# Kernel optimization log

Hardware: AMD Instinct MI355X
Metric: run time of the kernel (lower is better)

Reference implementation:

```python
import jax, jax.numpy as jnp
import numpy as np

N, E, ND, ED, HD = 50000, 800000, 64, 64, 192  # HD == 2*ND + ED (required by edge_gru)
NEG_SLOPE_BOOST = 0.2   # LeakyReLU inside msg_booster
NEG_SLOPE_OUT = 0.01    # F.leaky_relu default
LN_EPS = 1e-5


def leaky_relu(x, slope):
    return jnp.where(x > 0, x, slope * x)


def msg_booster(x, W1, b1, ln_g, ln_b, W2, b2):
    # Linear -> LayerNorm -> LeakyReLU(0.2) -> Linear
    y = x @ W1.T + b1
    mu = jnp.mean(y, axis=-1, keepdims=True)
    var = jnp.var(y, axis=-1, keepdims=True)
    y = (y - mu) * jax.lax.rsqrt(var + LN_EPS) * ln_g + ln_b
    y = leaky_relu(y, NEG_SLOPE_BOOST)
    return y @ W2.T + b2


def gru_cell(x, h, Wih, Whh, bih, bhh):
    gi = x @ Wih.T + bih
    gh = h @ Whh.T + bhh
    ir, iz, inn = jnp.split(gi, 3, axis=-1)
    hr, hz, hn = jnp.split(gh, 3, axis=-1)
    r = jax.nn.sigmoid(ir + hr)
    z = jax.nn.sigmoid(iz + hz)
    n = jnp.tanh(inn + r * hn)
    return (1.0 - z) * n + z * h


def setup_inputs() -> dict:
    key = jax.random.key(0)
    ks = jax.random.split(key, 24)
    r = lambda i, shape: jax.random.normal(ks[i], shape, dtype=jnp.float32) * 0.05
    return dict(
        node_feats=jax.random.normal(ks[0], (N, ND), dtype=jnp.float32),
        edge_feats=jax.random.normal(ks[1], (E, ED), dtype=jnp.float32),
        src=jax.random.randint(ks[2], (E,), 0, N),
        dst=jax.random.randint(ks[3], (E,), 0, N),
        W1e=r(4, (HD, 2 * ND + ED)),       # booster first linear, edge path
        W1n=r(5, (HD, 2 * (ND + ED))),     # booster first linear, node path
        b1=r(6, (HD,)),
        ln_g=jnp.ones((HD,), jnp.float32),
        ln_b=jnp.zeros((HD,), jnp.float32),
        W2=r(7, (HD, HD)), b2=r(8, (HD,)),
        Wih_e=r(9, (3 * ED, HD)), Whh_e=r(10, (3 * ED, ED)),
        bih_e=r(11, (3 * ED,)), bhh_e=r(12, (3 * ED,)),
        Wih_a=r(13, (3 * ND, HD)), Whh_a=r(14, (3 * ND, ND)),
        bih_a=r(15, (3 * ND,)), bhh_a=r(16, (3 * ND,)),
        Wre=r(17, (ED, ED)), bre=r(18, (ED,)),
        Wra=r(19, (ND, ND)), bra=r(20, (ND,)),
    )


def reference(node_feats, edge_feats, src, dst,
              W1e, W1n, b1, ln_g, ln_b, W2, b2,
              Wih_e, Whh_e, bih_e, bhh_e,
              Wih_a, Whh_a, bih_a, bhh_a,
              Wre, bre, Wra, bra):
    # --- edge update: gather src/dst node feats, concat with edge feats ---
    h_src = node_feats[src]                       # [E, ND]
    h_dst = node_feats[dst]                       # [E, ND]
    msg = jnp.concatenate([h_src, h_dst, edge_feats], axis=1)  # [E, 2ND+ED]
    edge_input = msg_booster(msg, W1e, b1, ln_g, ln_b, W2, b2)  # [E, HD]
    update_edges = leaky_relu(
        gru_cell(edge_input, edge_feats, Wih_e, Whh_e, bih_e, bhh_e)
        + edge_feats @ Wre.T + bre, NEG_SLOPE_OUT)              # [E, ED]

    # --- message passing: m = [h_src, e'] aggregated at dst by sum and max ---
    m = jnp.concatenate([h_src, update_edges], axis=1)          # [E, ND+ED]
    agg_sum = jax.ops.segment_sum(m, dst, num_segments=N)       # [N, ND+ED]
    agg_max = jax.ops.segment_max(m, dst, num_segments=N)
    agg_max = jnp.where(jnp.isfinite(agg_max), agg_max, 0.0)    # empty mailbox -> 0
    agg = jnp.concatenate([agg_sum, agg_max], axis=1)           # [N, 2(ND+ED)]

    node_input = msg_booster(agg, W1n, b1, ln_g, ln_b, W2, b2)  # [N, HD]
    update_nodes = leaky_relu(
        gru_cell(node_input, node_feats, Wih_a, Whh_a, bih_a, bhh_a)
        + node_feats @ Wra.T + bra, NEG_SLOPE_OUT)              # [N, ND]
    return update_nodes, update_edges
```

## Files before the change

### kernel.cpp

```cpp
#include <hip/hip_runtime.h>

#define NN 50000
#define EE 800000
#define ND 64
#define ED 64
#define HD 192
#define AS 196

typedef short s16x8 __attribute__((ext_vector_type(8)));
typedef float f32x4 __attribute__((ext_vector_type(4)));

#define MFMA16 __builtin_amdgcn_mfma_f32_16x16x32_bf16

__device__ __forceinline__ unsigned short bf16rn(float x) {
  unsigned u = __float_as_uint(x);
  return (unsigned short)((u + 0x7fffu + ((u >> 16) & 1u)) >> 16);
}

__device__ __forceinline__ void split8(const float* p, s16x8& hi, s16x8& lo) {
  f32x4 a = *(const f32x4*)p;
  f32x4 b = *(const f32x4*)(p + 4);
#pragma unroll
  for (int j = 0; j < 4; ++j) {
    unsigned short h = bf16rn(a[j]);
    float hf = __uint_as_float(((unsigned)h) << 16);
    unsigned short l = bf16rn(a[j] - hf);
    hi[j] = (short)h; lo[j] = (short)l;
  }
#pragma unroll
  for (int j = 0; j < 4; ++j) {
    unsigned short h = bf16rn(b[j]);
    float hf = __uint_as_float(((unsigned)h) << 16);
    unsigned short l = bf16rn(b[j] - hf);
    hi[4 + j] = (short)h; lo[4 + j] = (short)l;
  }
}

__device__ __forceinline__ float fsigmoid(float x) { return 1.f / (1.f + __expf(-x)); }
__device__ __forceinline__ float ftanh(float x) {
  const float ax = fabsf(x);
  const float t = __expf(2.f * ax);
  const float r = 1.f - 2.f / (t + 1.f);
  return x >= 0.f ? r : -r;
}

template <int NT, int KS, int NTOT = NT>
__device__ __forceinline__ void gemm3p(f32x4* acc, const s16x8* ah, const s16x8* al,
                                       const unsigned short* __restrict__ pack, int lane) {
  const int HOFF = NTOT * KS * 512;
#pragma unroll
  for (int ks = 0; ks < KS; ++ks) {
#pragma unroll
    for (int nt = 0; nt < NT; ++nt) {
      const unsigned short* bp = pack + ((nt * KS + ks) * 64 + lane) * 8;
      s16x8 bh = *(const s16x8*)bp;
      s16x8 bl = *(const s16x8*)(bp + HOFF);
      acc[nt] = MFMA16(ah[ks], bh, acc[nt], 0, 0, 0);
      acc[nt] = MFMA16(al[ks], bh, acc[nt], 0, 0, 0);
      acc[nt] = MFMA16(ah[ks], bl, acc[nt], 0, 0, 0);
    }
  }
}

__global__ void k_pack(const float* __restrict__ w0, const float* __restrict__ w1,
                       const float* __restrict__ w2, const float* __restrict__ w3,
                       const float* __restrict__ w4, const float* __restrict__ w5,
                       const float* __restrict__ w6, const float* __restrict__ w7,
                       const float* __restrict__ w8, unsigned short* __restrict__ packs) {
  int gid = blockIdx.x * 256 + threadIdx.x;
  const float* w; int off, sz, KS, K, local;
  if      (gid <  36864) { w = w0; off = 0;      sz = 36864; KS = 6; K = 192; local = gid; }
  else if (gid <  86016) { w = w1; off = 73728;  sz = 49152; KS = 8; K = 256; local = gid - 36864; }
  else if (gid < 122880) { w = w2; off = 172032; sz = 36864; KS = 6; K = 192; local = gid - 86016; }
  else if (gid < 159744) { w = w3; off = 245760; sz = 36864; KS = 6; K = 192; local = gid - 122880; }
  else if (gid < 172032) { w = w4; off = 319488; sz = 12288; KS = 2; K = 64;  local = gid - 159744; }
  else if (gid < 176128) { w = w5; off = 344064; sz = 4096;  KS = 2; K = 64;  local = gid - 172032; }
  else if (gid < 212992) { w = w6; off = 352256; sz = 36864; KS = 6; K = 192; local = gid - 176128; }
  else if (gid < 225280) { w = w7; off = 425984; sz = 12288; KS = 2; K = 64;  local = gid - 212992; }
  else                   { w = w8; off = 450560; sz = 4096;  KS = 2; K = 64;  local = gid - 225280; }
  int j = local & 7;
  int lane = (local >> 3) & 63;
  int t = local >> 9;
  int ks = t % KS, nt = t / KS;
  int n = nt * 16 + (lane & 15);
  int k = ks * 32 + ((lane >> 4) & 3) * 8 + j;
  float v = w[n * K + k];
  unsigned short h = bf16rn(v);
  float hf = __uint_as_float(((unsigned)h) << 16);
  unsigned short l = bf16rn(v - hf);
  packs[off + local] = h;
  packs[off + sz + local] = l;
}

__global__ void k_packfuse(const float* __restrict__ W2,
                           const float* __restrict__ WihE, const float* __restrict__ WihA,
                           unsigned short* __restrict__ packs) {
  int gid = blockIdx.x * 256 + threadIdx.x;
  const float* Wih; int off, local;
  if (gid < 36864) { Wih = WihE; off = 245760; local = gid; }
  else             { Wih = WihA; off = 352256; local = gid - 36864; }
  int j = local & 7;
  int lane = (local >> 3) & 63;
  int t = local >> 9;
  int ks = t % 6, nt = t / 6;
  int n = nt * 16 + (lane & 15);
  int k = ks * 32 + ((lane >> 4) & 3) * 8 + j;
  const float* wr = Wih + n * HD;
  float acc = 0.f;
#pragma unroll 4
  for (int jj = 0; jj < HD; ++jj) acc = fmaf(wr[jj], W2[jj * HD + k], acc);
  unsigned short h = bf16rn(acc);
  float hf = __uint_as_float(((unsigned)h) << 16);
  unsigned short l = bf16rn(acc - hf);
  packs[off + local] = h;
  packs[off + 36864 + local] = l;
}

__global__ void k_fusebias(const float* __restrict__ WihE, const float* __restrict__ WihA,
                           const float* __restrict__ b2, const float* __restrict__ bihE,
                           const float* __restrict__ bihA, float* __restrict__ bf) {
  int i = threadIdx.x;
  const float* Wih = (i < 192) ? WihE : WihA;
  const float* bih = (i < 192) ? bihE : bihA;
  int n = (i < 192) ? i : i - 192;
  float acc = bih[n];
  for (int k = 0; k < HD; ++k) acc = fmaf(Wih[n * HD + k], b2[k], acc);
  bf[i] = acc;
}

__global__ void k_zero(int* __restrict__ cnt) {
  int i = blockIdx.x * 256 + threadIdx.x;
  if (i < NN) cnt[i] = 0;
}
__global__ void k_hist(const int* __restrict__ dst, int* __restrict__ cnt) {
  int e = blockIdx.x * 256 + threadIdx.x;
  if (e < EE) atomicAdd(&cnt[dst[e]], 1);
}
__global__ void k_scan(const int* __restrict__ cnt, int* __restrict__ roff, int* __restrict__ cursor) {
  __shared__ int wsum[16];
  const int tid = threadIdx.x;
  const int lane = tid & 63, wid = tid >> 6;
  int carry = 0;
  for (int c = 0; c < 49; ++c) {
    const int idx = c * 1024 + tid;
    const int v = (idx < NN) ? cnt[idx] : 0;
    int x = v;
#pragma unroll
    for (int off = 1; off < 64; off <<= 1) {
      int y = __shfl_up(x, off, 64);
      if (lane >= off) x += y;
    }
    if (lane == 63) wsum[wid] = x;
    __syncthreads();
    if (wid == 0 && lane < 16) {
      int s = wsum[lane];
#pragma unroll
      for (int off = 1; off < 16; off <<= 1) {
        int y = __shfl_up(s, off, 16);
        if (lane >= off) s += y;
      }
      wsum[lane] = s;
    }
    __syncthreads();
    const int wbase = (wid == 0) ? 0 : wsum[wid - 1];
    const int excl = carry + wbase + x - v;
    if (idx < NN) { roff[idx] = excl; cursor[idx] = excl; }
    const int total = wsum[15];
    __syncthreads();
    carry += total;
  }
  if (tid == 0) roff[NN] = carry;
}
__global__ void k_scatter(const int* __restrict__ dst, int* __restrict__ cursor, int* __restrict__ elist) {
  int e = blockIdx.x * 256 + threadIdx.x;
  if (e < EE) {
    int p = atomicAdd(&cursor[dst[e]], 1);
    elist[p] = e;
  }
}

__global__ __launch_bounds__(256, 3)
void edge_kernel(const float* __restrict__ nf, const float* __restrict__ efg,
                 const int* __restrict__ src, const int* __restrict__ dst,
                 const float* __restrict__ b1, const float* __restrict__ lng,
                 const float* __restrict__ lnb,
                 const float* __restrict__ bfz, const float* __restrict__ bhh,
                 const float* __restrict__ bre,
                 const unsigned short* __restrict__ pW1,
                 const unsigned short* __restrict__ pWih, const unsigned short* __restrict__ pWhh,
                 const unsigned short* __restrict__ pWre,
                 float* __restrict__ oute) {
  __shared__ float act[64 * AS];
  const int tid = threadIdx.x;
  const int e0 = blockIdx.x * 64;

  {
    const int r = tid >> 2, q = tid & 3;
    const int s = src[e0 + r];
    const int d = dst[e0 + r];
    const f32x4* nf4 = (const f32x4*)nf;
    const f32x4* ef4 = (const f32x4*)efg;
#pragma unroll
    for (int i = 0; i < 4; ++i) {
      const int c4 = q * 4 + i;
      *(f32x4*)&act[r * AS + c4 * 4]       = nf4[s * 16 + c4];
      *(f32x4*)&act[r * AS + 64 + c4 * 4]  = nf4[d * 16 + c4];
      *(f32x4*)&act[r * AS + 128 + c4 * 4] = ef4[(e0 + r) * 16 + c4];
    }
  }
  __syncthreads();

  const int w = tid >> 6, lane = tid & 63;
  const int quad = lane >> 4, lc = lane & 15;
  const int arow = w * 16 + lc;
  const int obase = w * 16 + quad * 4;
  const f32x4 vzero = {0.f, 0.f, 0.f, 0.f};

  s16x8 ah[6], al[6];
  f32x4 acc[12];

#pragma unroll
  for (int ks = 0; ks < 6; ++ks) split8(&act[arow * AS + ks * 32 + quad * 8], ah[ks], al[ks]);
#pragma unroll
  for (int nt = 0; nt < 12; ++nt) acc[nt] = vzero;
  gemm3p<12, 6>(acc, ah, al, pW1, lane);
  {
    float s1[4] = {0, 0, 0, 0}, s2[4] = {0, 0, 0, 0};
#pragma unroll
    for (int nt = 0; nt < 12; ++nt) {
      const float bb = b1[nt * 16 + lc];
#pragma unroll
      for (int r = 0; r < 4; ++r) {
        const float v = acc[nt][r] + bb;
        acc[nt][r] = v; s1[r] += v; s2[r] += v * v;
      }
    }
#pragma unroll
    for (int r = 0; r < 4; ++r) {
#pragma unroll
      for (int m = 1; m < 16; m <<= 1) {
        s1[r] += __shfl_xor(s1[r], m, 16);
        s2[r] += __shfl_xor(s2[r], m, 16);
      }
      const float mu = s1[r] * (1.f / 192.f);
      const float va = s2[r] * (1.f / 192.f) - mu * mu;
      s1[r] = mu; s2[r] = rsqrtf(va + 1e-5f);
    }
#pragma unroll
    for (int nt = 0; nt < 12; ++nt) {
      const int col = nt * 16 + lc;
      const float g = lng[col], be = lnb[col];
#pragma unroll
      for (int r = 0; r < 4; ++r) {
        float v = (acc[nt][r] - s1[r]) * s2[r] * g + be;
        v = v > 0.f ? v : 0.2f * v;
        act[(obase + r) * AS + col] = v;
      }
    }
  }
  __syncthreads();

#pragma unroll
  for (int ks = 0; ks < 6; ++ks) split8(&act[arow * AS + ks * 32 + quad * 8], ah[ks], al[ks]);
  f32x4 rz[8], ni[4], nh[4], ro[4];
#pragma unroll
  for (int nt = 0; nt < 8; ++nt) rz[nt] = vzero;
#pragma unroll
  for (int nt = 0; nt < 4; ++nt) { ni[nt] = vzero; nh[nt] = vzero; ro[nt] = vzero; }
  gemm3p<8, 6, 12>(rz, ah, al, pWih, lane);
  gemm3p<4, 6, 12>(ni, ah, al, pWih + 8 * 6 * 512, lane);

  s16x8 eh[2], el[2];
#pragma unroll
  for (int ks = 0; ks < 2; ++ks)
    split8(efg + (size_t)(e0 + arow) * ED + ks * 32 + quad * 8, eh[ks], el[ks]);
  gemm3p<8, 2, 12>(rz, eh, el, pWhh, lane);
  gemm3p<4, 2, 12>(nh, eh, el, pWhh + 8 * 2 * 512, lane);
  gemm3p<4, 2>(ro, eh, el, pWre, lane);

#pragma unroll
  for (int nt = 0; nt < 4; ++nt) {
    const int col = nt * 16 + lc;
    const float bir = bfz[col], biz = bfz[64 + col], bin = bfz[128 + col];
    const float bhr = bhh[col], bhz = bhh[64 + col], bhn = bhh[128 + col];
    const float br = bre[col];
#pragma unroll
    for (int r = 0; r < 4; ++r) {
      const int row = obase + r;
      const float h = efg[(size_t)(e0 + row) * ED + col];
      const float rg = fsigmoid(rz[nt][r] + bir + bhr);
      const float zg = fsigmoid(rz[nt + 4][r] + biz + bhz);
      const float ng = ftanh(ni[nt][r] + bin + rg * (nh[nt][r] + bhn));
      float v = (1.f - zg) * ng + zg * h + ro[nt][r] + br;
      v = v > 0.f ? v : 0.01f * v;
      oute[(size_t)(e0 + row) * ED + col] = v;
    }
  }
}

__global__ __launch_bounds__(256, 2)
void node_kernel(const float* __restrict__ nf,
                 const int* __restrict__ src,
                 const int* __restrict__ roff, const int* __restrict__ elist,
                 const float* __restrict__ b1, const float* __restrict__ lng,
                 const float* __restrict__ lnb,
                 const float* __restrict__ bfz, const float* __restrict__ bhh,
                 const float* __restrict__ bra,
                 const unsigned short* __restrict__ pW1,
                 const unsigned short* __restrict__ pWih, const unsigned short* __restrict__ pWhh,
                 const unsigned short* __restrict__ pWra,
                 const float* __restrict__ upd,
                 float* __restrict__ outn) {
  __shared__ float act[4 * 4096];
  const int tid = threadIdx.x;
  const int w = tid >> 6, lane = tid & 63;
  const int nb0 = blockIdx.x * 64;
  float* win = act + w * 4096;

  {
    const int half = lane >> 5, c2 = (lane & 31) * 2;
#pragma unroll 1
    for (int i = 0; i < 16; ++i) {
      const int node = nb0 + w * 16 + i;
      float s0 = 0.f, s1v = 0.f;
      float m0 = -__builtin_inff(), m1 = -__builtin_inff();
      if (node < NN) {
        const int sidx = roff[node], eidx = roff[node + 1];
        int ix = sidx;
        for (; ix + 1 < eidx; ix += 2) {
          const int ea = elist[ix], eb = elist[ix + 1];
          const float* pa = half ? (upd + (size_t)ea * ED + c2) : (nf + (size_t)src[ea] * ND + c2);
          const float* pb = half ? (upd + (size_t)eb * ED + c2) : (nf + (size_t)src[eb] * ND + c2);
          const float a0 = pa[0], a1 = pa[1], c0 = pb[0], c1 = pb[1];
          s0 += a0 + c0; s1v += a1 + c1;
          m0 = fmaxf(m0, fmaxf(a0, c0)); m1 = fmaxf(m1, fmaxf(a1, c1));
        }
        if (ix < eidx) {
          const int ea = elist[ix];
          const float* pa = half ? (upd + (size_t)ea * ED + c2) : (nf + (size_t)src[ea] * ND + c2);
          const float a0 = pa[0], a1 = pa[1];
          s0 += a0; s1v += a1;
          m0 = fmaxf(m0, a0); m1 = fmaxf(m1, a1);
        }
        if (sidx == eidx) { m0 = 0.f; m1 = 0.f; }
      } else {
        m0 = 0.f; m1 = 0.f;
      }
      const int cs = half * 64 + c2;
      win[i * 256 + cs] = s0;
      win[i * 256 + cs + 1] = s1v;
      win[i * 256 + 128 + cs] = m0;
      win[i * 256 + 128 + cs + 1] = m1;
    }
  }
  __syncthreads();

  const int quad = lane >> 4, lc = lane & 15;
  const f32x4 vzero = {0.f, 0.f, 0.f, 0.f};

  s16x8 ah8[8], al8[8];
#pragma unroll
  for (int ks = 0; ks < 8; ++ks) split8(&win[lc * 256 + ks * 32 + quad * 8], ah8[ks], al8[ks]);
  f32x4 acc[12];
#pragma unroll
  for (int nt = 0; nt < 12; ++nt) acc[nt] = vzero;
  gemm3p<12, 8>(acc, ah8, al8, pW1, lane);
  {
    float s1[4] = {0, 0, 0, 0}, s2[4] = {0, 0, 0, 0};
#pragma unroll
    for (int nt = 0; nt < 12; ++nt) {
      const float bb = b1[nt * 16 + lc];
#pragma unroll
      for (int r = 0; r < 4; ++r) {
        const float v = acc[nt][r] + bb;
        acc[nt][r] = v; s1[r] += v; s2[r] += v * v;
      }
    }
#pragma unroll
    for (int r = 0; r < 4; ++r) {
#pragma unroll
      for (int m = 1; m < 16; m <<= 1) {
        s1[r] += __shfl_xor(s1[r], m, 16);
        s2[r] += __shfl_xor(s2[r], m, 16);
      }
      const float mu = s1[r] * (1.f / 192.f);
      const float va = s2[r] * (1.f / 192.f) - mu * mu;
      s1[r] = mu; s2[r] = rsqrtf(va + 1e-5f);
    }
#pragma unroll
    for (int nt = 0; nt < 12; ++nt) {
      const int col = nt * 16 + lc;
      const float g = lng[col], be = lnb[col];
#pragma unroll
      for (int r = 0; r < 4; ++r) {
        float v = (acc[nt][r] - s1[r]) * s2[r] * g + be;
        v = v > 0.f ? v : 0.2f * v;
        win[(quad * 4 + r) * AS + col] = v;
      }
    }
  }
  __syncthreads();

  s16x8 ah[6], al[6];
#pragma unroll
  for (int ks = 0; ks < 6; ++ks) split8(&win[lc * AS + ks * 32 + quad * 8], ah[ks], al[ks]);
  f32x4 rz[8], ni[4], nh[4], ro[4];
#pragma unroll
  for (int nt = 0; nt < 8; ++nt) rz[nt] = vzero;
#pragma unroll
  for (int nt = 0; nt < 4; ++nt) { ni[nt] = vzero; nh[nt] = vzero; ro[nt] = vzero; }
  gemm3p<8, 6, 12>(rz, ah, al, pWih, lane);
  gemm3p<4, 6, 12>(ni, ah, al, pWih + 8 * 6 * 512, lane);

  s16x8 hh[2], hl[2];
  {
    const int gr = nb0 + w * 16 + lc;
    const float* hp = nf + (size_t)(gr < NN ? gr : NN - 1) * ND;
#pragma unroll
    for (int ks = 0; ks < 2; ++ks) split8(hp + ks * 32 + quad * 8, hh[ks], hl[ks]);
  }
  gemm3p<8, 2, 12>(rz, hh, hl, pWhh, lane);
  gemm3p<4, 2, 12>(nh, hh, hl, pWhh + 8 * 2 * 512, lane);
  gemm3p<4, 2>(ro, hh, hl, pWra, lane);

#pragma unroll
  for (int nt = 0; nt < 4; ++nt) {
    const int col = nt * 16 + lc;
    const float bir = bfz[col], biz = bfz[64 + col], bin = bfz[128 + col];
    const float bhr = bhh[col], bhz = bhh[64 + col], bhn = bhh[128 + col];
    const float br = bra[col];
#pragma unroll
    for (int r = 0; r < 4; ++r) {
      const int node = nb0 + w * 16 + quad * 4 + r;
      if (node < NN) {
        const float h = nf[(size_t)node * ND + col];
        const float rg = fsigmoid(rz[nt][r] + bir + bhr);
        const float zg = fsigmoid(rz[nt + 4][r] + biz + bhz);
        const float ng = ftanh(ni[nt][r] + bin + rg * (nh[nt][r] + bhn));
        float v = (1.f - zg) * ng + zg * h + ro[nt][r] + br;
        v = v > 0.f ? v : 0.01f * v;
        outn[(size_t)node * ND + col] = v;
      }
    }
  }
}

extern "C" void kernel_launch(void* const* d_in, const int* in_sizes, int n_in,
                              void* d_out, int out_size, void* d_ws, size_t ws_size,
                              hipStream_t stream) {
  (void)in_sizes; (void)n_in; (void)out_size; (void)ws_size;
  const float* nf    = (const float*)d_in[0];
  const float* ef    = (const float*)d_in[1];
  const int*   src   = (const int*)d_in[2];
  const int*   dst   = (const int*)d_in[3];
  const float* W1e   = (const float*)d_in[4];
  const float* W1n   = (const float*)d_in[5];
  const float* b1    = (const float*)d_in[6];
  const float* lng   = (const float*)d_in[7];
  const float* lnb   = (const float*)d_in[8];
  const float* W2    = (const float*)d_in[9];
  const float* b2    = (const float*)d_in[10];
  const float* Wih_e = (const float*)d_in[11];
  const float* Whh_e = (const float*)d_in[12];
  const float* bih_e = (const float*)d_in[13];
  const float* bhh_e = (const float*)d_in[14];
  const float* Wih_a = (const float*)d_in[15];
  const float* Whh_a = (const float*)d_in[16];
  const float* bih_a = (const float*)d_in[17];
  const float* bhh_a = (const float*)d_in[18];
  const float* Wre   = (const float*)d_in[19];
  const float* bre   = (const float*)d_in[20];
  const float* Wra   = (const float*)d_in[21];
  const float* bra   = (const float*)d_in[22];

  unsigned short* packs = (unsigned short*)d_ws;
  char* base = (char*)d_ws;
  int* cnt    = (int*)(base + 917504);
  int* roff   = (int*)(base + 1117504);
  int* cursor = (int*)(base + 1317512);
  int* elist  = (int*)(base + 1517512);
  float* bfused = (float*)cursor;

  constexpr int OFF_W1e = 0, OFF_W1n = 73728,
                OFF_Wihe = 245760, OFF_Whhe = 319488, OFF_Wre = 344064,
                OFF_Wiha = 352256, OFF_Whha = 425984, OFF_Wra = 450560;

  float* out_nodes = (float*)d_out;
  float* out_edges = out_nodes + (size_t)NN * ND;

  k_pack<<<896, 256, 0, stream>>>(W1e, W1n, W2, Wih_e, Whh_e, Wre, Wih_a, Whh_a, Wra, packs);
  k_packfuse<<<288, 256, 0, stream>>>(W2, Wih_e, Wih_a, packs);
  k_zero<<<(NN + 255) / 256, 256, 0, stream>>>(cnt);
  k_hist<<<(EE + 255) / 256, 256, 0, stream>>>(dst, cnt);
  k_scan<<<1, 1024, 0, stream>>>(cnt, roff, cursor);
  k_scatter<<<(EE + 255) / 256, 256, 0, stream>>>(dst, cursor, elist);
  k_fusebias<<<1, 384, 0, stream>>>(Wih_e, Wih_a, b2, bih_e, bih_a, bfused);

  edge_kernel<<<EE / 64, 256, 0, stream>>>(
      nf, ef, src, dst, b1, lng, lnb, bfused, bhh_e, bre,
      packs + OFF_W1e, packs + OFF_Wihe, packs + OFF_Whhe, packs + OFF_Wre,
      out_edges);

  node_kernel<<<(NN + 63) / 64, 256, 0, stream>>>(
      nf, src, roff, elist, b1, lng, lnb, bfused + 192, bhh_a, bra,
      packs + OFF_W1n, packs + OFF_Wiha, packs + OFF_Whha, packs + OFF_Wra,
      out_edges, out_nodes);
}
```

Before: 1.814 ms.

## Split edge-kernel GEMM by output columns per wave and store activations pre-split

The edge kernel now has each wave compute a slice of output columns for all 64 rows, instead of all columns for its own 16 rows. Each weight fragment loaded from global memory is therefore reused across four row groups, cutting per-wave weight traffic. Activations are stored in shared memory as packed bf16 hi/lo pairs, so later GEMMs unpack them with byte permutes rather than re-splitting floats. LayerNorm statistics now need a cross-wave reduction through shared memory, which adds two barriers and more live accumulators, raising register pressure.

```diff
diff --git a/kernel.cpp b/kernel.cpp
--- a/kernel.cpp
+++ b/kernel.cpp
@@ -9,12 +9,36 @@
 
 typedef short s16x8 __attribute__((ext_vector_type(8)));
 typedef float f32x4 __attribute__((ext_vector_type(4)));
+typedef unsigned u32x4 __attribute__((ext_vector_type(4)));
 
 #define MFMA16 __builtin_amdgcn_mfma_f32_16x16x32_bf16
 
 __device__ __forceinline__ unsigned short bf16rn(float x) {
   unsigned u = __float_as_uint(x);
   return (unsigned short)((u + 0x7fffu + ((u >> 16) & 1u)) >> 16);
+}
+
+__device__ __forceinline__ unsigned packhl(float x) {
+  unsigned short h = bf16rn(x);
+  float hf = __uint_as_float(((unsigned)h) << 16);
+  unsigned short l = bf16rn(x - hf);
+  return (((unsigned)h) << 16) | l;
+}
+
+__device__ __forceinline__ void unpack8(const unsigned* p, s16x8& hi, s16x8& lo) {
+  u32x4 a = *(const u32x4*)p;
+  u32x4 b = *(const u32x4*)(p + 4);
+  u32x4 h, l;
+  h[0] = __builtin_amdgcn_perm(a[1], a[0], 0x07060302u);
+  h[1] = __builtin_amdgcn_perm(a[3], a[2], 0x07060302u);
+  h[2] = __builtin_amdgcn_perm(b[1], b[0], 0x07060302u);
+  h[3] = __builtin_amdgcn_perm(b[3], b[2], 0x07060302u);
+  l[0] = __builtin_amdgcn_perm(a[1], a[0], 0x05040100u);
+  l[1] = __builtin_amdgcn_perm(a[3], a[2], 0x05040100u);
+  l[2] = __builtin_amdgcn_perm(b[1], b[0], 0x05040100u);
+  l[3] = __builtin_amdgcn_perm(b[3], b[2], 0x05040100u);
+  hi = __builtin_bit_cast(s16x8, h);
+  lo = __builtin_bit_cast(s16x8, l);
 }
 
 __device__ __forceinline__ void split8(const float* p, s16x8& hi, s16x8& lo) {
@@ -44,6 +68,11 @@
   return x >= 0.f ? r : -r;
 }
 
+#define TRI(ACC, AH, AL, BH, BL)          \
+  ACC = MFMA16(AH, BH, ACC, 0, 0, 0);     \
+  ACC = MFMA16(AL, BH, ACC, 0, 0, 0);     \
+  ACC = MFMA16(AH, BL, ACC, 0, 0, 0);
+
 template <int NT, int KS, int NTOT = NT>
 __device__ __forceinline__ void gemm3p(f32x4* acc, const s16x8* ah, const s16x8* al,
                                        const unsigned short* __restrict__ pack, int lane) {
@@ -55,9 +84,7 @@
       const unsigned short* bp = pack + ((nt * KS + ks) * 64 + lane) * 8;
       s16x8 bh = *(const s16x8*)bp;
       s16x8 bl = *(const s16x8*)(bp + HOFF);
-      acc[nt] = MFMA16(ah[ks], bh, acc[nt], 0, 0, 0);
-      acc[nt] = MFMA16(al[ks], bh, acc[nt], 0, 0, 0);
-      acc[nt] = MFMA16(ah[ks], bl, acc[nt], 0, 0, 0);
+      TRI(acc[nt], ah[ks], al[ks], bh, bl);
     }
   }
 }
@@ -190,7 +217,9 @@
                  const unsigned short* __restrict__ pWih, const unsigned short* __restrict__ pWhh,
                  const unsigned short* __restrict__ pWre,
                  float* __restrict__ oute) {
-  __shared__ float act[64 * AS];
+  __shared__ unsigned actP[64 * AS];
+  __shared__ float lnPart[4 * 64 * 2];
+  __shared__ float lnFin[64 * 2];
   const int tid = threadIdx.x;
   const int e0 = blockIdx.x * 64;
 
@@ -203,98 +232,185 @@
 #pragma unroll
     for (int i = 0; i < 4; ++i) {
       const int c4 = q * 4 + i;
-      *(f32x4*)&act[r * AS + c4 * 4]       = nf4[s * 16 + c4];
-      *(f32x4*)&act[r * AS + 64 + c4 * 4]  = nf4[d * 16 + c4];
-      *(f32x4*)&act[r * AS + 128 + c4 * 4] = ef4[(e0 + r) * 16 + c4];
+      f32x4 a = nf4[s * 16 + c4];
+      f32x4 b = nf4[d * 16 + c4];
+      f32x4 c = ef4[(e0 + r) * 16 + c4];
+      u32x4 pa, pb, pc;
+#pragma unroll
+      for (int j = 0; j < 4; ++j) {
+        pa[j] = packhl(a[j]); pb[j] = packhl(b[j]); pc[j] = packhl(c[j]);
+      }
+      *(u32x4*)&actP[r * AS + c4 * 4]       = pa;
+      *(u32x4*)&actP[r * AS + 64 + c4 * 4]  = pb;
+      *(u32x4*)&actP[r * AS + 128 + c4 * 4] = pc;
     }
   }
   __syncthreads();
 
   const int w = tid >> 6, lane = tid & 63;
   const int quad = lane >> 4, lc = lane & 15;
-  const int arow = w * 16 + lc;
-  const int obase = w * 16 + quad * 4;
   const f32x4 vzero = {0.f, 0.f, 0.f, 0.f};
 
-  s16x8 ah[6], al[6];
-  f32x4 acc[12];
-
-#pragma unroll
-  for (int ks = 0; ks < 6; ++ks) split8(&act[arow * AS + ks * 32 + quad * 8], ah[ks], al[ks]);
-#pragma unroll
-  for (int nt = 0; nt < 12; ++nt) acc[nt] = vzero;
-  gemm3p<12, 6>(acc, ah, al, pW1, lane);
+  f32x4 acc[3][4];
+#pragma unroll
+  for (int s = 0; s < 3; ++s)
+#pragma unroll
+    for (int g = 0; g < 4; ++g) acc[s][g] = vzero;
+#pragma unroll
+  for (int ks = 0; ks < 6; ++ks) {
+    s16x8 ah4[4], al4[4];
+#pragma unroll
+    for (int g = 0; g < 4; ++g)
+      unpack8(&actP[(g * 16 + lc) * AS + ks * 32 + quad * 8], ah4[g], al4[g]);
+#pragma unroll
+    for (int s = 0; s < 3; ++s) {
+      const unsigned short* bp = pW1 + (((w + s * 4) * 6 + ks) * 64 + lane) * 8;
+      s16x8 bh = *(const s16x8*)bp;
+      s16x8 bl = *(const s16x8*)(bp + 36864);
+#pragma unroll
+      for (int g = 0; g < 4; ++g) { TRI(acc[s][g], ah4[g], al4[g], bh, bl); }
+    }
+  }
+
   {
-    float s1[4] = {0, 0, 0, 0}, s2[4] = {0, 0, 0, 0};
-#pragma unroll
-    for (int nt = 0; nt < 12; ++nt) {
-      const float bb = b1[nt * 16 + lc];
+    float p1[16], p2[16];
+#pragma unroll
+    for (int i = 0; i < 16; ++i) { p1[i] = 0.f; p2[i] = 0.f; }
+#pragma unroll
+    for (int s = 0; s < 3; ++s) {
+      const float bb = b1[(w + s * 4) * 16 + lc];
+#pragma unroll
+      for (int g = 0; g < 4; ++g)
+#pragma unroll
+        for (int r = 0; r < 4; ++r) {
+          const float v = acc[s][g][r] + bb;
+          acc[s][g][r] = v;
+          p1[g * 4 + r] += v; p2[g * 4 + r] += v * v;
+        }
+    }
+#pragma unroll
+    for (int i = 0; i < 16; ++i) {
+#pragma unroll
+      for (int m = 1; m < 16; m <<= 1) {
+        p1[i] += __shfl_xor(p1[i], m, 16);
+        p2[i] += __shfl_xor(p2[i], m, 16);
+      }
+    }
+    if (lc == 0) {
+#pragma unroll
+      for (int g = 0; g < 4; ++g)
+#pragma unroll
+        for (int r = 0; r < 4; ++r) {
+          const int row = g * 16 + quad * 4 + r;
+          lnPart[(w * 64 + row) * 2]     = p1[g * 4 + r];
+          lnPart[(w * 64 + row) * 2 + 1] = p2[g * 4 + r];
+        }
+    }
+  }
+  __syncthreads();
+
+  if (lane < 16) {
+    const int row = w * 16 + lane;
+    float s1 = 0.f, s2 = 0.f;
+#pragma unroll
+    for (int wv = 0; wv < 4; ++wv) {
+      s1 += lnPart[(wv * 64 + row) * 2];
+      s2 += lnPart[(wv * 64 + row) * 2 + 1];
+    }
+    const float mu = s1 * (1.f / 192.f);
+    const float va = s2 * (1.f / 192.f) - mu * mu;
+    lnFin[row * 2] = mu;
+    lnFin[row * 2 + 1] = rsqrtf(va + 1e-5f);
+  }
+  __syncthreads();
+
+  {
+    float gg[3], be[3];
+#pragma unroll
+    for (int s = 0; s < 3; ++s) {
+      const int col = (w + s * 4) * 16 + lc;
+      gg[s] = lng[col]; be[s] = lnb[col];
+    }
+#pragma unroll
+    for (int g = 0; g < 4; ++g)
 #pragma unroll
       for (int r = 0; r < 4; ++r) {
-        const float v = acc[nt][r] + bb;
-        acc[nt][r] = v; s1[r] += v; s2[r] += v * v;
-      }
-    }
-#pragma unroll
-    for (int r = 0; r < 4; ++r) {
-#pragma unroll
-      for (int m = 1; m < 16; m <<= 1) {
-        s1[r] += __shfl_xor(s1[r], m, 16);
-        s2[r] += __shfl_xor(s2[r], m, 16);
-      }
-      const float mu = s1[r] * (1.f / 192.f);
-      const float va = s2[r] * (1.f / 192.f) - mu * mu;
-      s1[r] = mu; s2[r] = rsqrtf(va + 1e-5f);
-    }
-#pragma unroll
-    for (int nt = 0; nt < 12; ++nt) {
-      const int col = nt * 16 + lc;
-      const float g = lng[col], be = lnb[col];
-#pragma unroll
-      for (int r = 0; r < 4; ++r) {
-        float v = (acc[nt][r] - s1[r]) * s2[r] * g + be;
-        v = v > 0.f ? v : 0.2f * v;
-        act[(obase + r) * AS + col] = v;
-      }
-    }
+        const int row = g * 16 + quad * 4 + r;
+        const float mu = lnFin[row * 2], rsig = lnFin[row * 2 + 1];
+#pragma unroll
+        for (int s = 0; s < 3; ++s) {
+          float v = (acc[s][g][r] - mu) * rsig * gg[s] + be[s];
+          v = v > 0.f ? v : 0.2f * v;
+          actP[row * AS + (w + s * 4) * 16 + lc] = packhl(v);
+        }
+      }
   }
   __syncthreads();
 
-#pragma unroll
-  for (int ks = 0; ks < 6; ++ks) split8(&act[arow * AS + ks * 32 + quad * 8], ah[ks], al[ks]);
-  f32x4 rz[8], ni[4], nh[4], ro[4];
-#pragma unroll
-  for (int nt = 0; nt < 8; ++nt) rz[nt] = vzero;
-#pragma unroll
-  for (int nt = 0; nt < 4; ++nt) { ni[nt] = vzero; nh[nt] = vzero; ro[nt] = vzero; }
-  gemm3p<8, 6, 12>(rz, ah, al, pWih, lane);
-  gemm3p<4, 6, 12>(ni, ah, al, pWih + 8 * 6 * 512, lane);
-
-  s16x8 eh[2], el[2];
-#pragma unroll
-  for (int ks = 0; ks < 2; ++ks)
-    split8(efg + (size_t)(e0 + arow) * ED + ks * 32 + quad * 8, eh[ks], el[ks]);
-  gemm3p<8, 2, 12>(rz, eh, el, pWhh, lane);
-  gemm3p<4, 2, 12>(nh, eh, el, pWhh + 8 * 2 * 512, lane);
-  gemm3p<4, 2>(ro, eh, el, pWre, lane);
-
-#pragma unroll
-  for (int nt = 0; nt < 4; ++nt) {
-    const int col = nt * 16 + lc;
+  f32x4 rza[2][4], ni4[4], nh4[4], ro4[4];
+#pragma unroll
+  for (int g = 0; g < 4; ++g) {
+    rza[0][g] = vzero; rza[1][g] = vzero; ni4[g] = vzero; nh4[g] = vzero; ro4[g] = vzero;
+  }
+#pragma unroll
+  for (int ks = 0; ks < 6; ++ks) {
+    s16x8 ah4[4], al4[4];
+#pragma unroll
+    for (int g = 0; g < 4; ++g)
+      unpack8(&actP[(g * 16 + lc) * AS + ks * 32 + quad * 8], ah4[g], al4[g]);
+#pragma unroll
+    for (int s = 0; s < 3; ++s) {
+      const unsigned short* bp = pWih + (((w + s * 4) * 6 + ks) * 64 + lane) * 8;
+      s16x8 bh = *(const s16x8*)bp;
+      s16x8 bl = *(const s16x8*)(bp + 36864);
+      f32x4* dst_acc = (s == 0) ? &rza[0][0] : (s == 1) ? &rza[1][0] : &ni4[0];
+#pragma unroll
+      for (int g = 0; g < 4; ++g) { TRI(dst_acc[g], ah4[g], al4[g], bh, bl); }
+    }
+  }
+
+#pragma unroll
+  for (int ks = 0; ks < 2; ++ks) {
+    s16x8 eh4[4], el4[4];
+#pragma unroll
+    for (int g = 0; g < 4; ++g)
+      split8(efg + (size_t)(e0 + g * 16 + lc) * ED + ks * 32 + quad * 8, eh4[g], el4[g]);
+#pragma unroll
+    for (int s = 0; s < 3; ++s) {
+      const unsigned short* bp = pWhh + (((w + s * 4) * 2 + ks) * 64 + lane) * 8;
+      s16x8 bh = *(const s16x8*)bp;
+      s16x8 bl = *(const s16x8*)(bp + 12288);
+      f32x4* dst_acc = (s == 0) ? &rza[0][0] : (s == 1) ? &rza[1][0] : &nh4[0];
+#pragma unroll
+      for (int g = 0; g < 4; ++g) { TRI(dst_acc[g], eh4[g], el4[g], bh, bl); }
+    }
+    {
+      const unsigned short* bp = pWre + ((w * 2 + ks) * 64 + lane) * 8;
+      s16x8 bh = *(const s16x8*)bp;
+      s16x8 bl = *(const s16x8*)(bp + 4096);
+#pragma unroll
+      for (int g = 0; g < 4; ++g) { TRI(ro4[g], eh4[g], el4[g], bh, bl); }
+    }
+  }
+
+  {
+    const int col = w * 16 + lc;
     const float bir = bfz[col], biz = bfz[64 + col], bin = bfz[128 + col];
     const float bhr = bhh[col], bhz = bhh[64 + col], bhn = bhh[128 + col];
     const float br = bre[col];
 #pragma unroll
-    for (int r = 0; r < 4; ++r) {
-      const int row = obase + r;
-      const float h = efg[(size_t)(e0 + row) * ED + col];
-      const float rg = fsigmoid(rz[nt][r] + bir + bhr);
-      const float zg = fsigmoid(rz[nt + 4][r] + biz + bhz);
-      const float ng = ftanh(ni[nt][r] + bin + rg * (nh[nt][r] + bhn));
-      float v = (1.f - zg) * ng + zg * h + ro[nt][r] + br;
-      v = v > 0.f ? v : 0.01f * v;
-      oute[(size_t)(e0 + row) * ED + col] = v;
-    }
+    for (int g = 0; g < 4; ++g)
+#pragma unroll
+      for (int r = 0; r < 4; ++r) {
+        const int row = g * 16 + quad * 4 + r;
+        const float h = efg[(size_t)(e0 + row) * ED + col];
+        const float rgate = fsigmoid(rza[0][g][r] + bir + bhr);
+        const float zgate = fsigmoid(rza[1][g][r] + biz + bhz);
+        const float ngate = ftanh(ni4[g][r] + bin + rgate * (nh4[g][r] + bhn));
+        float v = (1.f - zgate) * ngate + zgate * h + ro4[g][r] + br;
+        v = v > 0.f ? v : 0.01f * v;
+        oute[(size_t)(e0 + row) * ED + col] = v;
+      }
   }
 }
 
```

Result: faster. 1.489 ms (-17.9%).
